# Optimization experiments

Measured on AMD Instinct MI355X. Metric: run time of the kernel, lower is better.

## Reference

```python
import jax, jax.numpy as jnp
import numpy as np

NUM_HEADS = 12
HEAD_DIM = 64


def setup_inputs() -> dict:
    key = jax.random.key(0)
    ks = jax.random.split(key, 8)
    B, S, D, M = 8, 1024, 768, 8
    scale = 0.02
    return {
        "hidden_states": jax.random.normal(ks[0], (B, S, D), jnp.float32),
        "memory": jax.random.normal(ks[1], (1, M, D), jnp.float32) * scale,
        "Wq": jax.random.normal(ks[2], (D, D), jnp.float32) * scale,
        "bq": jnp.zeros((D,), jnp.float32),
        "Wk": jax.random.normal(ks[3], (D, D), jnp.float32) * scale,
        "bk": jnp.zeros((D,), jnp.float32),
        "Wv": jax.random.normal(ks[4], (D, D), jnp.float32) * scale,
        "bv": jnp.zeros((D,), jnp.float32),
    }


def _split_heads(x):
    # (B, S, D) -> (B, H, S, Dh)
    B, S, _ = x.shape
    return x.reshape(B, S, NUM_HEADS, HEAD_DIM).transpose(0, 2, 1, 3)


def reference(hidden_states, memory, Wq, bq, Wk, bk, Wv, bv):
    B, S, D = hidden_states.shape
    # prepend? no: memory tokens are concatenated AFTER hidden_states on token dim
    mem = jnp.broadcast_to(memory, (B,) + memory.shape[1:])
    with_memory = jnp.concatenate([hidden_states, mem], axis=1)  # (B, S+M, D)

    # torch nn.Linear: x @ W.T + b
    q = _split_heads(hidden_states @ Wq.T + bq)   # (B, H, S,   Dh)
    k = _split_heads(with_memory @ Wk.T + bk)     # (B, H, S+M, Dh)
    v = _split_heads(with_memory @ Wv.T + bv)     # (B, H, S+M, Dh)

    scaling = 1.0 / np.sqrt(HEAD_DIM).astype(np.float32)
    scores = jnp.einsum("bhqd,bhkd->bhqk", q, k) * scaling
    probs = jax.nn.softmax(scores, axis=-1)  # dropout is identity in eval
    ctx = jnp.einsum("bhqk,bhkd->bhqd", probs, v)  # (B, H, S, Dh)
    ctx = ctx.transpose(0, 2, 1, 3).reshape(B, S, D)
    return ctx
```

## Files before the change

kernel.cpp:

```cpp
#include <hip/hip_runtime.h>

typedef unsigned short ushort_t;
typedef __attribute__((ext_vector_type(8))) short bf16x8;
typedef __attribute__((ext_vector_type(4))) short s16x4;
typedef __attribute__((ext_vector_type(4))) float f32x4;

#define BATCH 8
#define SEQ   1024
#define MEMT  8
#define LREAL 1032
#define LPAD  1152
#define DMODEL 768
#define NH    12
#define DH    64

#define CEXP 0.18033688011112042f

__device__ __forceinline__ ushort_t f2b(float x) {
  union { float f; unsigned u; } c; c.f = x;
  unsigned u = c.u;
  unsigned r = (u + 0x7fffu + ((u >> 16) & 1u)) >> 16;
  return (ushort_t)r;
}

#if defined(__has_builtin)
#if __has_builtin(__builtin_amdgcn_global_load_lds)
#define HAVE_GLL 1
#endif
#if __has_builtin(__builtin_amdgcn_exp2f)
#define EXP2F(x) __builtin_amdgcn_exp2f(x)
#endif
#endif
#ifndef EXP2F
#define EXP2F(x) __expf((x) * 0.6931471805599453f)
#endif

__device__ __forceinline__ void stage16(const ushort_t* g, ushort_t* lds_wave_base) {
#ifdef HAVE_GLL
  __builtin_amdgcn_global_load_lds(
      (const __attribute__((address_space(1))) unsigned int*)g,
      (__attribute__((address_space(3))) unsigned int*)lds_wave_base,
      16, 0, 0);
#else
  int lane = threadIdx.x & 63;
  *(bf16x8*)(lds_wave_base + lane * 8) = *(const bf16x8*)g;
#endif
}

__global__ __launch_bounds__(256) void prep(const float* __restrict__ hidden,
                                            const float* __restrict__ memv,
                                            const float* __restrict__ Wq,
                                            const float* __restrict__ Wk,
                                            const float* __restrict__ Wv,
                                            ushort_t* __restrict__ Xm,
                                            ushort_t* __restrict__ Wqb,
                                            ushort_t* __restrict__ Wkb,
                                            ushort_t* __restrict__ Wvb) {
  int bx = blockIdx.x;
  if (bx < 6912) {
    size_t idx = ((size_t)bx * 256 + threadIdx.x) * 4;
    const size_t perB = (size_t)LPAD * DMODEL;
    int b = (int)(idx / perB);
    size_t rem = idx - (size_t)b * perB;
    int row = (int)(rem / DMODEL);
    int col = (int)(rem - (size_t)row * DMODEL);
    f32x4 v;
    if (row < SEQ) {
      v = *(const f32x4*)(hidden + ((size_t)b * SEQ + row) * DMODEL + col);
    } else if (row < LREAL) {
      v = *(const f32x4*)(memv + (size_t)(row - SEQ) * DMODEL + col);
    } else {
      v = (f32x4){0.f, 0.f, 0.f, 0.f};
    }
    s16x4 p;
    p[0] = (short)f2b(v[0]); p[1] = (short)f2b(v[1]);
    p[2] = (short)f2b(v[2]); p[3] = (short)f2b(v[3]);
    *(s16x4*)(Xm + idx) = p;
  } else {
    int t = bx - 6912;
    int m = t / 576;
    int i = (t - m * 576) * 256 + threadIdx.x;
    const float* src = m == 0 ? Wq : (m == 1 ? Wk : Wv);
    ushort_t* dst = m == 0 ? Wqb : (m == 1 ? Wkb : Wvb);
    f32x4 v = *(const f32x4*)(src + (size_t)i * 4);
    s16x4 p;
    p[0] = (short)f2b(v[0]); p[1] = (short)f2b(v[1]);
    p[2] = (short)f2b(v[2]); p[3] = (short)f2b(v[3]);
    *(s16x4*)(dst + (size_t)i * 4) = p;
  }
}

__global__ __launch_bounds__(256) void gemm_fused(
    const ushort_t* __restrict__ Xm,
    const ushort_t* __restrict__ Wqb, const ushort_t* __restrict__ Wkb,
    const ushort_t* __restrict__ Wvb,
    const float* __restrict__ bq, const float* __restrict__ bk,
    const float* __restrict__ bv,
    ushort_t* __restrict__ Qb, ushort_t* __restrict__ Kb,
    ushort_t* __restrict__ Vtb) {
  __shared__ __align__(16) ushort_t As[2 * 4096];
  __shared__ __align__(16) ushort_t Bs[2 * 4096];
  const int tid = threadIdx.x;
  const int wave = tid >> 6, lane = tid & 63;
  const int quad = lane >> 4, l15 = lane & 15;
  const int wm = wave >> 1, wn = wave & 1;

  int bx = blockIdx.x;
  int task, xt, yt, b;
  if (bx < 432) {
    int slot = bx & 7, rest = bx >> 3;
    int y = rest % 6, vhi = rest / 6;
    int v = slot + 8 * vhi;
    task = 2; xt = v % 9; b = v / 9; yt = y;
  } else if (bx < 816) {
    int t = bx - 432;
    int slot = t & 7, rest = t >> 3;
    int x = rest % 6, qhi = rest / 6;
    int q = slot + 8 * qhi;
    task = 0; xt = x; yt = q & 7; b = q >> 3;
  } else {
    int t = bx - 816;
    int slot = t & 7, rest = t >> 3;
    int x = rest % 6, khi = rest / 6;
    int k = slot + 8 * khi;
    task = 1; xt = x; yt = k % 9; b = k / 9;
  }
  const int rowTile = yt * 128, colTile = xt * 128;
  const ushort_t* Xb = Xm + (size_t)b * LPAD * DMODEL;
  const ushort_t* A = task == 2 ? Wvb : Xb;
  const ushort_t* W = task == 2 ? Xb : (task == 0 ? Wqb : Wkb);
  const float* bias = task == 2 ? bv : (task == 0 ? bq : bk);

  const int srow = tid >> 2;
  const int scol = (tid & 3) << 3;

  f32x4 acc[4][4] = {};

  for (int k0 = 0; k0 < DMODEL; k0 += 64) {
#pragma unroll
    for (int kk = 0; kk < 2; ++kk)
#pragma unroll
      for (int is = 0; is < 2; ++is) {
        int r = is * 64 + srow;
        int lb = kk * 4096 + is * 2048 + wave * 512;
        stage16(A + (size_t)(rowTile + r) * DMODEL + k0 + kk * 32 + scol, As + lb);
        stage16(W + (size_t)(colTile + r) * DMODEL + k0 + kk * 32 + scol, Bs + lb);
      }
    __syncthreads();
#pragma unroll
    for (int kk = 0; kk < 2; ++kk) {
      bf16x8 af[4], bfr[4];
#pragma unroll
      for (int mt = 0; mt < 4; ++mt)
        af[mt] = *(const bf16x8*)&As[kk * 4096 + (wm * 64 + mt * 16 + l15) * 32 + quad * 8];
#pragma unroll
      for (int nt = 0; nt < 4; ++nt)
        bfr[nt] = *(const bf16x8*)&Bs[kk * 4096 + (wn * 64 + nt * 16 + l15) * 32 + quad * 8];
#pragma unroll
      for (int mt = 0; mt < 4; ++mt)
#pragma unroll
        for (int nt = 0; nt < 4; ++nt)
          acc[mt][nt] = __builtin_amdgcn_mfma_f32_16x16x32_bf16(af[mt], bfr[nt], acc[mt][nt], 0, 0, 0);
    }
    __syncthreads();
  }

  if (task == 2) {
#pragma unroll
    for (int mt = 0; mt < 4; ++mt) {
      int row0 = rowTile + wm * 64 + mt * 16 + quad * 4;
      float bvr[4];
#pragma unroll
      for (int r = 0; r < 4; ++r) bvr[r] = bias[row0 + r];
#pragma unroll
      for (int nt = 0; nt < 4; ++nt) {
        int col = colTile + wn * 64 + nt * 16 + l15;
#pragma unroll
        for (int r = 0; r < 4; ++r) {
          int row = row0 + r;
          Vtb[(((size_t)b * NH + (row >> 6)) * DH + (row & 63)) * LPAD + col] =
              f2b(acc[mt][nt][r] + bvr[r]);
        }
      }
    }
  } else {
    ushort_t* out = task == 0 ? Qb : Kb;
    const int Rows = task == 0 ? SEQ : LPAD;
    const float scale = task == 0 ? CEXP : 1.0f;
#pragma unroll
    for (int mt = 0; mt < 4; ++mt)
#pragma unroll
      for (int nt = 0; nt < 4; ++nt) {
        int row0 = rowTile + wm * 64 + mt * 16 + quad * 4;
        int col = colTile + wn * 64 + nt * 16 + l15;
        int h = col >> 6, d = col & 63;
        float bsv = bias[col];
#pragma unroll
        for (int r = 0; r < 4; ++r)
          out[(((size_t)b * NH + h) * Rows + (row0 + r)) * DH + d] =
              f2b((acc[mt][nt][r] + bsv) * scale);
      }
  }
}

__global__ __launch_bounds__(256, 3) void attn(const ushort_t* __restrict__ Q,
                                               const ushort_t* __restrict__ K,
                                               const ushort_t* __restrict__ Vt,
                                               float* __restrict__ Out) {
  __shared__ __align__(16) ushort_t Ks[2 * 4096];
  __shared__ __align__(16) ushort_t Vs[4 * 2048];
  __shared__ __align__(16) ushort_t Ps[4 * 2304];

  const int tid = threadIdx.x, wave = tid >> 6, lane = tid & 63;
  const int quad = lane >> 4, l15 = lane & 15;
  const int bh = blockIdx.x, qt = blockIdx.y;
  const int h = bh % NH, b = bh / NH;

  const ushort_t* Qp = Q + (((size_t)b * NH + h) * SEQ + qt * 128) * DH;
  const ushort_t* Kp = K + ((size_t)b * NH + h) * LPAD * DH;
  const ushort_t* Vp = Vt + ((size_t)b * NH + h) * DH * LPAD;
  ushort_t* Pw = Ps + wave * 2304;

  bf16x8 qf[2][2];
#pragma unroll
  for (int mt = 0; mt < 2; ++mt)
#pragma unroll
    for (int kk = 0; kk < 2; ++kk)
      qf[mt][kk] = *(const bf16x8*)&Qp[(wave * 32 + mt * 16 + l15) * DH + kk * 32 + quad * 8];

  bf16x8 ones8;
#pragma unroll
  for (int j = 0; j < 8; ++j) ones8[j] = (short)0x3f80;

  f32x4 ob[2][4] = {};
  f32x4 obl[2] = {};

  const int srow = tid >> 2;
  const int scol = (tid & 3) << 3;

  for (int kt = 0; kt < 9; ++kt) {
    const int key0 = kt * 128;
#pragma unroll
    for (int kk = 0; kk < 2; ++kk)
#pragma unroll
      for (int is = 0; is < 2; ++is) {
        int krow = is * 64 + srow;
        stage16(Kp + (size_t)(key0 + krow) * DH + kk * 32 + scol,
                Ks + kk * 4096 + is * 2048 + wave * 512);
      }
#pragma unroll
    for (int kc = 0; kc < 4; ++kc)
      stage16(Vp + (size_t)srow * LPAD + key0 + kc * 32 + scol,
              Vs + kc * 2048 + wave * 512);
    __syncthreads();

#pragma unroll
    for (int half = 0; half < 2; ++half) {
      f32x4 sc[2][4] = {};
#pragma unroll
      for (int kk = 0; kk < 2; ++kk)
#pragma unroll
        for (int nt = 0; nt < 4; ++nt) {
          bf16x8 kf = *(const bf16x8*)&Ks[kk * 4096 + (half * 64 + nt * 16 + l15) * 32 + quad * 8];
#pragma unroll
          for (int mt = 0; mt < 2; ++mt)
            sc[mt][nt] = __builtin_amdgcn_mfma_f32_16x16x32_bf16(qf[mt][kk], kf, sc[mt][nt], 0, 0, 0);
        }

      if (kt < 8) {
#pragma unroll
        for (int mt = 0; mt < 2; ++mt)
#pragma unroll
          for (int nt = 0; nt < 4; ++nt)
#pragma unroll
            for (int r = 0; r < 4; ++r) {
              union { float f; unsigned u; } cu;
              cu.f = EXP2F(sc[mt][nt][r]);
              Pw[(mt * 16 + quad * 4 + r) * 72 + nt * 16 + l15] = (ushort_t)(cu.u >> 16);
            }
      } else {
#pragma unroll
        for (int mt = 0; mt < 2; ++mt)
#pragma unroll
          for (int nt = 0; nt < 4; ++nt) {
            int key = key0 + half * 64 + nt * 16 + l15;
            bool valid = key < LREAL;
#pragma unroll
            for (int r = 0; r < 4; ++r) {
              union { float f; unsigned u; } cu;
              cu.f = valid ? EXP2F(sc[mt][nt][r]) : 0.f;
              Pw[(mt * 16 + quad * 4 + r) * 72 + nt * 16 + l15] = (ushort_t)(cu.u >> 16);
            }
          }
      }

#pragma unroll
      for (int kc2 = 0; kc2 < 2; ++kc2) {
        int kcg = half * 2 + kc2;
        bf16x8 pf[2];
#pragma unroll
        for (int mt = 0; mt < 2; ++mt)
          pf[mt] = *(const bf16x8*)&Pw[(mt * 16 + l15) * 72 + kc2 * 32 + quad * 8];
#pragma unroll
        for (int dt = 0; dt < 4; ++dt) {
          bf16x8 vf = *(const bf16x8*)&Vs[kcg * 2048 + (dt * 16 + l15) * 32 + quad * 8];
#pragma unroll
          for (int mt = 0; mt < 2; ++mt)
            ob[mt][dt] = __builtin_amdgcn_mfma_f32_16x16x32_bf16(pf[mt], vf, ob[mt][dt], 0, 0, 0);
        }
#pragma unroll
        for (int mt = 0; mt < 2; ++mt)
          obl[mt] = __builtin_amdgcn_mfma_f32_16x16x32_bf16(pf[mt], ones8, obl[mt], 0, 0, 0);
      }
    }
    __syncthreads();
  }

#pragma unroll
  for (int mt = 0; mt < 2; ++mt) {
    int row0 = qt * 128 + wave * 32 + mt * 16 + quad * 4;
    f32x4 linv;
#pragma unroll
    for (int r = 0; r < 4; ++r) linv[r] = 1.0f / obl[mt][r];
#pragma unroll
    for (int dt = 0; dt < 4; ++dt) {
      int col = h * DH + dt * 16 + l15;
#pragma unroll
      for (int r = 0; r < 4; ++r)
        Out[((size_t)b * SEQ + row0 + r) * DMODEL + col] = ob[mt][dt][r] * linv[r];
    }
  }
}

extern "C" void kernel_launch(void* const* d_in, const int* in_sizes, int n_in,
                              void* d_out, int out_size, void* d_ws, size_t ws_size,
                              hipStream_t stream) {
  const float* hidden = (const float*)d_in[0];
  const float* memv   = (const float*)d_in[1];
  const float* Wq = (const float*)d_in[2];
  const float* bq = (const float*)d_in[3];
  const float* Wk = (const float*)d_in[4];
  const float* bk = (const float*)d_in[5];
  const float* Wv = (const float*)d_in[6];
  const float* bv = (const float*)d_in[7];
  float* out = (float*)d_out;

  char* ws = (char*)d_ws;
  size_t off = 0;
  ushort_t* Xm  = (ushort_t*)(ws + off); off += (size_t)BATCH * LPAD * DMODEL * 2;
  ushort_t* Wqb = (ushort_t*)(ws + off); off += (size_t)DMODEL * DMODEL * 2;
  ushort_t* Wkb = (ushort_t*)(ws + off); off += (size_t)DMODEL * DMODEL * 2;
  ushort_t* Wvb = (ushort_t*)(ws + off); off += (size_t)DMODEL * DMODEL * 2;
  ushort_t* Qb  = (ushort_t*)(ws + off); off += (size_t)BATCH * NH * SEQ * DH * 2;
  ushort_t* Kb  = (ushort_t*)(ws + off); off += (size_t)BATCH * NH * LPAD * DH * 2;
  ushort_t* Vtb = (ushort_t*)(ws + off);

  prep<<<dim3(8640), 256, 0, stream>>>(hidden, memv, Wq, Wk, Wv, Xm, Wqb, Wkb, Wvb);
  gemm_fused<<<dim3(1248), 256, 0, stream>>>(Xm, Wqb, Wkb, Wvb, bq, bk, bv, Qb, Kb, Vtb);
  attn<<<dim3(96, 8), 256, 0, stream>>>(Qb, Kb, Vtb, out);
}
```

Measured before the change: 186.1 us.

## Use 512-thread GEMM blocks and stage output tile through LDS for vectorized stores

The QKV projection GEMM now runs with 8 waves per block instead of 4, so each wave computes a 64x32 sub-tile and register pressure per wave drops. The epilogue writes the 128x128 bf16 tile into padded shared memory first, then each thread stores 64 contiguous bytes to global memory. This replaces scattered 2-byte stores, notably the transposed V writes. The cost is an extra LDS round trip and barrier, plus a larger shared allocation that may limit occupancy.

```diff
diff --git a/kernel.cpp b/kernel.cpp
--- a/kernel.cpp
+++ b/kernel.cpp
@@ -90,7 +90,7 @@
   }
 }
 
-__global__ __launch_bounds__(256) void gemm_fused(
+__global__ __launch_bounds__(512, 4) void gemm_fused(
     const ushort_t* __restrict__ Xm,
     const ushort_t* __restrict__ Wqb, const ushort_t* __restrict__ Wkb,
     const ushort_t* __restrict__ Wvb,
@@ -98,12 +98,14 @@
     const float* __restrict__ bv,
     ushort_t* __restrict__ Qb, ushort_t* __restrict__ Kb,
     ushort_t* __restrict__ Vtb) {
-  __shared__ __align__(16) ushort_t As[2 * 4096];
-  __shared__ __align__(16) ushort_t Bs[2 * 4096];
+  __shared__ __align__(16) ushort_t S[17408];
+  ushort_t* As = S;
+  ushort_t* Bs = S + 8192;
+
   const int tid = threadIdx.x;
   const int wave = tid >> 6, lane = tid & 63;
   const int quad = lane >> 4, l15 = lane & 15;
-  const int wm = wave >> 1, wn = wave & 1;
+  const int wm = wave >> 2, wn = wave & 3;
 
   int bx = blockIdx.x;
   int task, xt, yt, b;
@@ -131,75 +133,80 @@
   const ushort_t* W = task == 2 ? Xb : (task == 0 ? Wqb : Wkb);
   const float* bias = task == 2 ? bv : (task == 0 ? bq : bk);
 
-  const int srow = tid >> 2;
-  const int scol = (tid & 3) << 3;
-
-  f32x4 acc[4][4] = {};
+  const int lrow4 = lane >> 2, lcol8 = (lane & 3) << 3;
+
+  f32x4 acc[4][2] = {};
 
   for (int k0 = 0; k0 < DMODEL; k0 += 64) {
 #pragma unroll
-    for (int kk = 0; kk < 2; ++kk)
-#pragma unroll
-      for (int is = 0; is < 2; ++is) {
-        int r = is * 64 + srow;
-        int lb = kk * 4096 + is * 2048 + wave * 512;
-        stage16(A + (size_t)(rowTile + r) * DMODEL + k0 + kk * 32 + scol, As + lb);
-        stage16(W + (size_t)(colTile + r) * DMODEL + k0 + kk * 32 + scol, Bs + lb);
-      }
+    for (int s = 0; s < 4; ++s) {
+      int u = wave * 4 + s;
+      int x = u & 15;
+      int kk = x >> 3, rg = x & 7;
+      int lb = kk * 4096 + rg * 512;
+      if (u < 16) {
+        stage16(A + (size_t)(rowTile + rg * 16 + lrow4) * DMODEL + k0 + kk * 32 + lcol8,
+                As + lb);
+      } else {
+        stage16(W + (size_t)(colTile + rg * 16 + lrow4) * DMODEL + k0 + kk * 32 + lcol8,
+                Bs + lb);
+      }
+    }
     __syncthreads();
 #pragma unroll
     for (int kk = 0; kk < 2; ++kk) {
-      bf16x8 af[4], bfr[4];
+      bf16x8 af[4], bfr[2];
 #pragma unroll
       for (int mt = 0; mt < 4; ++mt)
         af[mt] = *(const bf16x8*)&As[kk * 4096 + (wm * 64 + mt * 16 + l15) * 32 + quad * 8];
 #pragma unroll
-      for (int nt = 0; nt < 4; ++nt)
-        bfr[nt] = *(const bf16x8*)&Bs[kk * 4096 + (wn * 64 + nt * 16 + l15) * 32 + quad * 8];
+      for (int nt = 0; nt < 2; ++nt)
+        bfr[nt] = *(const bf16x8*)&Bs[kk * 4096 + (wn * 32 + nt * 16 + l15) * 32 + quad * 8];
 #pragma unroll
       for (int mt = 0; mt < 4; ++mt)
 #pragma unroll
-        for (int nt = 0; nt < 4; ++nt)
+        for (int nt = 0; nt < 2; ++nt)
           acc[mt][nt] = __builtin_amdgcn_mfma_f32_16x16x32_bf16(af[mt], bfr[nt], acc[mt][nt], 0, 0, 0);
     }
     __syncthreads();
   }
 
-  if (task == 2) {
-#pragma unroll
-    for (int mt = 0; mt < 4; ++mt) {
-      int row0 = rowTile + wm * 64 + mt * 16 + quad * 4;
-      float bvr[4];
-#pragma unroll
-      for (int r = 0; r < 4; ++r) bvr[r] = bias[row0 + r];
-#pragma unroll
-      for (int nt = 0; nt < 4; ++nt) {
-        int col = colTile + wn * 64 + nt * 16 + l15;
-#pragma unroll
-        for (int r = 0; r < 4; ++r) {
-          int row = row0 + r;
-          Vtb[(((size_t)b * NH + (row >> 6)) * DH + (row & 63)) * LPAD + col] =
-              f2b(acc[mt][nt][r] + bvr[r]);
-        }
-      }
-    }
-  } else {
-    ushort_t* out = task == 0 ? Qb : Kb;
-    const int Rows = task == 0 ? SEQ : LPAD;
-    const float scale = task == 0 ? CEXP : 1.0f;
-#pragma unroll
-    for (int mt = 0; mt < 4; ++mt)
-#pragma unroll
-      for (int nt = 0; nt < 4; ++nt) {
-        int row0 = rowTile + wm * 64 + mt * 16 + quad * 4;
-        int col = colTile + wn * 64 + nt * 16 + l15;
-        int h = col >> 6, d = col & 63;
-        float bsv = bias[col];
-#pragma unroll
-        for (int r = 0; r < 4; ++r)
-          out[(((size_t)b * NH + h) * Rows + (row0 + r)) * DH + d] =
-              f2b((acc[mt][nt][r] + bsv) * scale);
-      }
+  const float scale = task == 0 ? CEXP : 1.0f;
+#pragma unroll
+  for (int mt = 0; mt < 4; ++mt)
+#pragma unroll
+    for (int nt = 0; nt < 2; ++nt) {
+      int lr0 = wm * 64 + mt * 16 + quad * 4;
+      int lc = wn * 32 + nt * 16 + l15;
+#pragma unroll
+      for (int r = 0; r < 4; ++r) {
+        float bsv = (task == 2) ? bias[rowTile + lr0 + r] : bias[colTile + lc];
+        S[(lr0 + r) * 136 + lc] = f2b((acc[mt][nt][r] + bsv) * scale);
+      }
+    }
+  __syncthreads();
+
+  {
+    int row = tid >> 2;
+    int segu = (tid & 3) * 32;
+    bf16x8 v0 = *(const bf16x8*)&S[row * 136 + segu + 0];
+    bf16x8 v1 = *(const bf16x8*)&S[row * 136 + segu + 8];
+    bf16x8 v2 = *(const bf16x8*)&S[row * 136 + segu + 16];
+    bf16x8 v3 = *(const bf16x8*)&S[row * 136 + segu + 24];
+    if (task == 2) {
+      int d = rowTile + row;
+      ushort_t* gp = Vtb + (((size_t)b * NH + (d >> 6)) * DH + (d & 63)) * LPAD + colTile + segu;
+      *(bf16x8*)(gp + 0) = v0;  *(bf16x8*)(gp + 8) = v1;
+      *(bf16x8*)(gp + 16) = v2; *(bf16x8*)(gp + 24) = v3;
+    } else {
+      ushort_t* out = task == 0 ? Qb : Kb;
+      const int Rows = task == 0 ? SEQ : LPAD;
+      int colbase = colTile + segu;
+      int h = colbase >> 6, dd = colbase & 63;
+      ushort_t* gp = out + (((size_t)b * NH + h) * Rows + rowTile + row) * DH + dd;
+      *(bf16x8*)(gp + 0) = v0;  *(bf16x8*)(gp + 8) = v1;
+      *(bf16x8*)(gp + 16) = v2; *(bf16x8*)(gp + 24) = v3;
+    }
   }
 }
 
@@ -356,6 +363,6 @@
   ushort_t* Vtb = (ushort_t*)(ws + off);
 
   prep<<<dim3(8640), 256, 0, stream>>>(hidden, memv, Wq, Wk, Wv, Xm, Wqb, Wkb, Wvb);
-  gemm_fused<<<dim3(1248), 256, 0, stream>>>(Xm, Wqb, Wkb, Wvb, bq, bk, bv, Qb, Kb, Vtb);
+  gemm_fused<<<dim3(1248), 512, 0, stream>>>(Xm, Wqb, Wkb, Wvb, bq, bk, bv, Qb, Kb, Vtb);
   attn<<<dim3(96, 8), 256, 0, stream>>>(Qb, Kb, Vtb, out);
 }
```

Result: no change. 185.6 us (-0.3%).
